# Optimization experiments

Measured on AMD Instinct MI355X. Metric: run time of the kernel, lower is better.

## Reference

```python
import jax, jax.numpy as jnp
import numpy as np

MAX_NUM_LEVELS = 3.5
NUM_LEVELS = 4  # mip levels 0..3 (levels clamped to [0, 2.5])


def affine_grid(matrix, N, H, W):
    # F.affine_grid, align_corners=False. matrix: (N,2,3) -> grid (N,H,W,2) in xy order.
    xs = (jnp.arange(W, dtype=jnp.float32) + 0.5) * (2.0 / W) - 1.0
    ys = (jnp.arange(H, dtype=jnp.float32) + 0.5) * (2.0 / H) - 1.0
    gy, gx = jnp.meshgrid(ys, xs, indexing='ij')
    base = jnp.stack([gx, gy, jnp.ones_like(gx)], axis=-1)  # (H,W,3)
    return jnp.einsum('hwk,nik->nhwi', base, matrix)  # (N,H,W,2)


def grid_sample_border(img, grid):
    # bilinear grid_sample, padding_mode='border', align_corners=False
    N, C, H, W = img.shape
    x = (grid[..., 0] + 1.0) * (W / 2.0) - 0.5
    y = (grid[..., 1] + 1.0) * (H / 2.0) - 0.5
    x0 = jnp.floor(x); y0 = jnp.floor(y)
    tx = x - x0; ty = y - y0
    x0i = jnp.clip(x0.astype(jnp.int32), 0, W - 1)
    x1i = jnp.clip(x0.astype(jnp.int32) + 1, 0, W - 1)
    y0i = jnp.clip(y0.astype(jnp.int32), 0, H - 1)
    y1i = jnp.clip(y0.astype(jnp.int32) + 1, 0, H - 1)
    b = jnp.arange(N)[:, None, None]
    g = lambda yi, xi: img[b, :, yi, xi]  # (N,Ho,Wo,C) gather
    out = (g(y0i, x0i) * ((1 - tx) * (1 - ty))[..., None]
           + g(y0i, x1i) * (tx * (1 - ty))[..., None]
           + g(y1i, x0i) * ((1 - tx) * ty)[..., None]
           + g(y1i, x1i) * (tx * ty)[..., None])
    return jnp.transpose(out, (0, 3, 1, 2))  # (N,C,Ho,Wo)


def blur_downsample(x):
    N, C, H, W = x.shape
    k1 = jnp.array([1., 3., 3., 1.], dtype=x.dtype) / 8.0
    k = k1[:, None] * k1[None, :]
    xp = jnp.pad(x, ((0, 0), (0, 0), (1, 2), (1, 2)), mode='reflect')
    kernel = jnp.broadcast_to(k[None, None], (C, 1, 4, 4))
    return jax.lax.conv_general_dilated(xp, kernel, window_strides=(2, 2), padding='VALID',
                                        feature_group_count=C,
                                        dimension_numbers=('NCHW', 'OIHW', 'NCHW'))


def compute_levels(grid, H, W):
    # per-pixel mip LOD from local stretch of the sampling grid (in source pixel units)
    coords = (grid + 1.0) * 0.5 * jnp.array([W, H], dtype=grid.dtype)  # (N,Ho,Wo,2)
    dx = coords[:, :-1, 1:] - coords[:, :-1, :-1]
    dy = coords[:, 1:, :-1] - coords[:, :-1, :-1]
    scale = jnp.maximum(jnp.linalg.norm(dx, axis=-1), jnp.linalg.norm(dy, axis=-1))
    scale = jnp.pad(scale, ((0, 0), (0, 1), (0, 1)), mode='edge')  # (N,Ho,Wo)
    levels = jnp.log2(jnp.maximum(scale, 1.0))
    return jnp.clip(levels, 0.0, MAX_NUM_LEVELS - 1.0)


def mipmap_warp(img, grid):
    N, C, H, W = img.shape
    levels = compute_levels(grid, H, W)  # (N,Ho,Wo)
    pyr = [img]
    for _ in range(NUM_LEVELS - 1):
        pyr.append(blur_downsample(pyr[-1]))
    samples = jnp.stack([grid_sample_border(p, grid) for p in pyr], axis=0)  # (L,N,C,Ho,Wo)
    ls = jnp.arange(NUM_LEVELS, dtype=levels.dtype)[:, None, None, None]
    w = jnp.clip(1.0 - jnp.abs(levels[None] - ls), 0.0, 1.0)  # trilinear blend weights (L,N,Ho,Wo)
    return jnp.einsum('lnhw,lnchw->nchw', w, samples)


def setup_inputs() -> dict:
    key = jax.random.key(0)
    k1, k2, k3 = jax.random.split(key, 3)
    N, C, H, W, D = 64, 3, 256, 256, 512
    img = jax.random.normal(k1, (N, C, H, W), dtype=jnp.float32)
    features = jax.random.normal(k2, (N, D), dtype=jnp.float32)
    # learned head params (zero-init in torch; small random here so the warp is nontrivial)
    lin_w = jax.random.normal(k3, (4, D), dtype=jnp.float32) * 0.02
    lin_b = jnp.zeros((4,), dtype=jnp.float32)
    return {'img': img, 'features': features, 'lin_w': lin_w, 'lin_b': lin_b}


def reference(img, features, lin_w, lin_b):
    params = features @ lin_w.T + lin_b  # (N,4)
    rot = jnp.tanh(params[:, 0:1]) * jnp.pi
    scale = jnp.exp(params[:, 1:2])
    sx, sy = params[:, 2:3], params[:, 3:4]
    c, s = jnp.cos(rot), jnp.sin(rot)
    matrix = jnp.concatenate([scale * c, -scale * s, sx, scale * s, scale * c, sy], axis=1).reshape(-1, 2, 3)
    affine_params = jnp.concatenate([rot, scale, sx, sy], axis=1)
    N, C, H, W = img.shape
    grid = affine_grid(matrix, N, H, W)
    out = mipmap_warp(img, grid)
    return out, grid, matrix, affine_params
```

## Files before the change

### kernel.cpp

```cpp
#include <hip/hip_runtime.h>
#include <math.h>

#define N_B 64
#define C_CH 3
#define H_IMG 256
#define W_IMG 256
#define D_FEAT 512

#define OUT_OFF_GRID   12582912
#define OUT_OFF_MATRIX 20971520
#define OUT_OFF_AFFINE 20971904

#define PYR1_SZ (N_B * 128 * 128 * 3)
#define PYR2_SZ (N_B * 64 * 64 * 3)
#define PYR3_SZ (N_B * 32 * 32 * 3)

typedef float v2f __attribute__((ext_vector_type(2)));
typedef float f4u __attribute__((ext_vector_type(4), aligned(4)));
typedef float f2u __attribute__((ext_vector_type(2), aligned(4)));

__global__ void params_kernel(const float* __restrict__ features,
                              const float* __restrict__ lin_w,
                              const float* __restrict__ lin_b,
                              float* __restrict__ out_matrix,
                              float* __restrict__ out_affine,
                              float* __restrict__ ws_params)
{
    const int n = blockIdx.x;
    const int t = threadIdx.x;
    const float* f = features + n * D_FEAT;
    float f0 = f[t];
    float f1 = f[t + 256];
    float a0 = f0 * lin_w[0 * D_FEAT + t] + f1 * lin_w[0 * D_FEAT + t + 256];
    float a1 = f0 * lin_w[1 * D_FEAT + t] + f1 * lin_w[1 * D_FEAT + t + 256];
    float a2 = f0 * lin_w[2 * D_FEAT + t] + f1 * lin_w[2 * D_FEAT + t + 256];
    float a3 = f0 * lin_w[3 * D_FEAT + t] + f1 * lin_w[3 * D_FEAT + t + 256];

    __shared__ float red[4][256];
    red[0][t] = a0; red[1][t] = a1; red[2][t] = a2; red[3][t] = a3;
    __syncthreads();
    for (int s = 128; s > 0; s >>= 1) {
        if (t < s) {
            red[0][t] += red[0][t + s];
            red[1][t] += red[1][t + s];
            red[2][t] += red[2][t + s];
            red[3][t] += red[3][t + s];
        }
        __syncthreads();
    }
    if (t == 0) {
        float p0 = red[0][0] + lin_b[0];
        float p1 = red[1][0] + lin_b[1];
        float p2 = red[2][0] + lin_b[2];
        float p3 = red[3][0] + lin_b[3];
        float rot   = tanhf(p0) * 3.14159265358979323846f;
        float scale = expf(p1);
        float c = cosf(rot), s = sinf(rot);
        float m00 = scale * c, m01 = -scale * s, m02 = p2;
        float m10 = scale * s, m11 =  scale * c, m12 = p3;
        out_matrix[n * 6 + 0] = m00;
        out_matrix[n * 6 + 1] = m01;
        out_matrix[n * 6 + 2] = m02;
        out_matrix[n * 6 + 3] = m10;
        out_matrix[n * 6 + 4] = m11;
        out_matrix[n * 6 + 5] = m12;
        out_affine[n * 4 + 0] = rot;
        out_affine[n * 4 + 1] = scale;
        out_affine[n * 4 + 2] = p2;
        out_affine[n * 4 + 3] = p3;
        float lv = log2f(fmaxf(scale, 1.0f));
        lv = fminf(fmaxf(lv, 0.0f), 2.5f);
        ws_params[n * 8 + 0] = m00;
        ws_params[n * 8 + 1] = m01;
        ws_params[n * 8 + 2] = m02;
        ws_params[n * 8 + 3] = m10;
        ws_params[n * 8 + 4] = m11;
        ws_params[n * 8 + 5] = m12;
        ws_params[n * 8 + 6] = lv;
        ws_params[n * 8 + 7] = 0.0f;
    }
}

__global__ void down1_kernel(const float* __restrict__ img,
                             float* __restrict__ pyr1,
                             const float* __restrict__ ws_params)
{
    const int n = blockIdx.y;
    if (ws_params[n * 8 + 6] <= 0.0f) return;
    const int idx = blockIdx.x * 256 + threadIdx.x;
    const int t = idx & 31;
    const int i = idx >> 5;

    int r[4];
#pragma unroll
    for (int a = 0; a < 4; a++) {
        int q = 2 * i + a - 1;
        if (q < 0) q = -q;
        if (q >= 256) q = 510 - q;
        r[a] = q;
    }
    const int c8 = 8 * t;
    const int li = (t > 0)  ? c8 - 1 : 1;
    const int ri = (t < 31) ? c8 + 8 : 254;

    const float* s = img + (size_t)n * 3 * 65536;

    const float k0 = 0.125f, k1 = 0.375f;
    const float kr[4] = {0.125f, 0.375f, 0.375f, 0.125f};

    float acc[3][4] = {};
#pragma unroll
    for (int a = 0; a < 4; a++) {
        const float* rbase = s + (size_t)r[a] * 256;
        f4u A[3], B[3];
        float L[3], R[3];
#pragma unroll
        for (int c = 0; c < 3; c++) {
            const float* row = rbase + c * 65536;
            A[c] = *(const f4u*)(row + c8);
            B[c] = *(const f4u*)(row + c8 + 4);
            L[c] = row[li];
            R[c] = row[ri];
        }
#pragma unroll
        for (int c = 0; c < 3; c++) {
            float h0 = k0 * L[c]   + k1 * A[c].x + k1 * A[c].y + k0 * A[c].z;
            float h1 = k0 * A[c].y + k1 * A[c].z + k1 * A[c].w + k0 * B[c].x;
            float h2 = k0 * A[c].w + k1 * B[c].x + k1 * B[c].y + k0 * B[c].z;
            float h3 = k0 * B[c].y + k1 * B[c].z + k1 * B[c].w + k0 * R[c];
            acc[c][0] += kr[a] * h0;
            acc[c][1] += kr[a] * h1;
            acc[c][2] += kr[a] * h2;
            acc[c][3] += kr[a] * h3;
        }
    }
    float* d = pyr1 + (size_t)n * (128 * 128 * 3) + ((size_t)i * 128 + 4 * t) * 3;
    f4u s0 = {acc[0][0], acc[1][0], acc[2][0], acc[0][1]};
    f4u s1 = {acc[1][1], acc[2][1], acc[0][2], acc[1][2]};
    f4u s2 = {acc[2][2], acc[0][3], acc[1][3], acc[2][3]};
    *(f4u*)(d)     = s0;
    *(f4u*)(d + 4) = s1;
    *(f4u*)(d + 8) = s2;
}

template<int Hs, int Ws>
__global__ void downN_kernel(const float* __restrict__ src,
                             float* __restrict__ dst,
                             const float* __restrict__ ws_params,
                             float lvl_gate)
{
    const int n = blockIdx.y;
    if (ws_params[n * 8 + 6] <= lvl_gate) return;
    constexpr int Hd = Hs / 2, Wd = Ws / 2;
    const int p = blockIdx.x * 256 + threadIdx.x;
    const int i = p / Wd;
    const int j = p % Wd;

    int r[4], cc[4];
#pragma unroll
    for (int a = 0; a < 4; a++) {
        int q = 2 * i + a - 1;
        if (q < 0) q = -q;
        if (q >= Hs) q = 2 * Hs - 2 - q;
        r[a] = q;
        int u = 2 * j + a - 1;
        if (u < 0) u = -u;
        if (u >= Ws) u = 2 * Ws - 2 - u;
        cc[a] = u;
    }
    const float* s = src + (size_t)n * 3 * Hs * Ws;
    const int rs = 3 * Ws;

    f4u T[4][4];
#pragma unroll
    for (int a = 0; a < 4; a++)
#pragma unroll
        for (int b = 0; b < 4; b++)
            T[a][b] = *(const f4u*)(s + r[a] * rs + 3 * cc[b]);

    const float k0 = 0.125f, k1 = 0.375f;
    const float kr[4] = {0.125f, 0.375f, 0.375f, 0.125f};
    float o[3];
#pragma unroll
    for (int c = 0; c < 3; c++) {
        float acc = 0.0f;
#pragma unroll
        for (int a = 0; a < 4; a++) {
            float h = k0 * T[a][0][c] + k1 * T[a][1][c]
                    + k1 * T[a][2][c] + k0 * T[a][3][c];
            acc += kr[a] * h;
        }
        o[c] = acc;
    }
    float* d = dst + (size_t)n * 3 * Hd * Wd + (size_t)p * 3;
    d[0] = o[0]; d[1] = o[1]; d[2] = o[2];
}

struct TapSetup {
    const float* row0;
    const float* row1;
    float w00, w01, w10, w11;
    bool selHi0, selLo1;
    size_t planeStride;
};

__device__ __forceinline__ TapSetup make_taps(const float* __restrict__ base, int l,
                                              float X, float Y)
{
    const int Wl = W_IMG >> l;
    const int Hl = H_IMG >> l;
    float x = (X + 1.0f) * (0.5f * (float)Wl) - 0.5f;
    float y = (Y + 1.0f) * (0.5f * (float)Hl) - 0.5f;
    float x0f = floorf(x), y0f = floorf(y);
    float tx = x - x0f, ty = y - y0f;
    int x0 = (int)x0f, y0 = (int)y0f;
    int y0i = min(max(y0,     0), Hl - 1);
    int y1i = min(max(y0 + 1, 0), Hl - 1);
    int xp = min(max(x0, 0), Wl - 2);
    TapSetup ts;
    ts.row0 = base + (size_t)y0i * Wl + xp;
    ts.row1 = base + (size_t)y1i * Wl + xp;
    ts.selHi0 = (x0 >= Wl - 1);
    ts.selLo1 = (x0 < 0);
    ts.w00 = (1.0f - tx) * (1.0f - ty);
    ts.w01 = tx * (1.0f - ty);
    ts.w10 = (1.0f - tx) * ty;
    ts.w11 = tx * ty;
    ts.planeStride = (size_t)Hl * Wl;
    return ts;
}

__device__ __forceinline__ float tap_eval(const TapSetup& ts, float2 a, float2 b)
{
    float t00 = ts.selHi0 ? a.y : a.x;
    float t01 = ts.selLo1 ? a.x : a.y;
    float t10 = ts.selHi0 ? b.y : b.x;
    float t11 = ts.selLo1 ? b.x : b.y;
    return ts.w00 * t00 + ts.w01 * t01 + ts.w10 * t10 + ts.w11 * t11;
}

struct NTap {
    const float* r0;
    const float* r1;
    float w00, w01, w10, w11;
    bool hi, lo;
};

__device__ __forceinline__ NTap make_ntap(const float* __restrict__ base, int l,
                                          float X, float Y)
{
    const int Wl = W_IMG >> l;
    const int Hl = H_IMG >> l;
    float x = (X + 1.0f) * (0.5f * (float)Wl) - 0.5f;
    float y = (Y + 1.0f) * (0.5f * (float)Hl) - 0.5f;
    float x0f = floorf(x), y0f = floorf(y);
    float tx = x - x0f, ty = y - y0f;
    int x0 = (int)x0f, y0 = (int)y0f;
    int y0i = min(max(y0,     0), Hl - 1);
    int y1i = min(max(y0 + 1, 0), Hl - 1);
    int xp  = min(max(x0, 0), Wl - 2);
    const int rs = 3 * Wl;
    NTap t;
    t.r0 = base + (size_t)y0i * rs + 3 * xp;
    t.r1 = base + (size_t)y1i * rs + 3 * xp;
    t.hi = (x0 >= Wl - 1);
    t.lo = (x0 < 0);
    t.w00 = (1.0f - tx) * (1.0f - ty);
    t.w01 = tx * (1.0f - ty);
    t.w10 = (1.0f - tx) * ty;
    t.w11 = tx * ty;
    return t;
}

struct NPay { f4u a; f2u a2; f4u b; f2u b2; };

__device__ __forceinline__ NPay ntap_load(const NTap& t)
{
    NPay p;
    p.a  = *(const f4u*)t.r0;  p.a2 = *(const f2u*)(t.r0 + 4);
    p.b  = *(const f4u*)t.r1;  p.b2 = *(const f2u*)(t.r1 + 4);
    return p;
}

__device__ __forceinline__ void ntap_eval(const NTap& t, const NPay& p, float* v)
{
    float e0[6] = {p.a.x, p.a.y, p.a.z, p.a.w, p.a2.x, p.a2.y};
    float e1[6] = {p.b.x, p.b.y, p.b.z, p.b.w, p.b2.x, p.b2.y};
#pragma unroll
    for (int c = 0; c < 3; c++) {
        float p00 = t.hi ? e0[c + 3] : e0[c];
        float p01 = t.lo ? e0[c]     : e0[c + 3];
        float p10 = t.hi ? e1[c + 3] : e1[c];
        float p11 = t.lo ? e1[c]     : e1[c + 3];
        v[c] = t.w00 * p00 + t.w01 * p01 + t.w10 * p10 + t.w11 * p11;
    }
}

__device__ __forceinline__ const float* npyr(int l, const float* p1,
                                             const float* p2, const float* p3,
                                             int n)
{
    if (l == 1) return p1 + (size_t)n * (128 * 128 * 3);
    if (l == 2) return p2 + (size_t)n * (64 * 64 * 3);
    return p3 + (size_t)n * (32 * 32 * 3);
}

__global__ __launch_bounds__(256, 4)
void warp_kernel(const float* __restrict__ img,
                 const float* __restrict__ pyr1,
                 const float* __restrict__ pyr2,
                 const float* __restrict__ pyr3,
                 const float* __restrict__ ws_params,
                 float* __restrict__ out,
                 float* __restrict__ gridOut)
{
    const int n = blockIdx.y;
    const int tile = blockIdx.x;
    const int tid = threadIdx.x;
    const int w0 = (tile & 7) << 5;
    const int h0 = (tile >> 3) << 4;
    const int w  = w0 + (((tid >> 6) & 1) << 4) + (tid & 15);
    const int ha = h0 + ((tid >> 7) << 2) + ((tid >> 4) & 3);
    const int hb = ha + 8;

    const float* P = ws_params + n * 8;
    float m00 = P[0], m01 = P[1], m02 = P[2];
    float m10 = P[3], m11 = P[4], m12 = P[5];
    float lv  = P[6];

    float gx  = ((float)w + 0.5f) * (2.0f / (float)W_IMG) - 1.0f;
    float gya = ((float)ha + 0.5f) * (2.0f / (float)H_IMG) - 1.0f;
    float gyb = ((float)hb + 0.5f) * (2.0f / (float)H_IMG) - 1.0f;
    float Xa = m00 * gx + m01 * gya + m02;
    float Ya = m10 * gx + m11 * gya + m12;
    float Xb = m00 * gx + m01 * gyb + m02;
    float Yb = m10 * gx + m11 * gyb + m12;

    v2f gpa = {Xa, Ya}, gpb = {Xb, Yb};
    __builtin_nontemporal_store(gpa, (v2f*)gridOut + ((size_t)(n * H_IMG + ha) * W_IMG + w));
    __builtin_nontemporal_store(gpb, (v2f*)gridOut + ((size_t)(n * H_IMG + hb) * W_IMG + w));

    int   l0   = (int)lv;
    float frac = lv - (float)l0;
    const bool hasL1 = (frac > 0.0f);
    const float wA = 1.0f - frac;

    size_t oba = ((size_t)n * C_CH * H_IMG + ha) * W_IMG + w;
    size_t obb = ((size_t)n * C_CH * H_IMG + hb) * W_IMG + w;

    if (l0 == 0) {
        const float* base0 = img + (size_t)n * 3 * 65536;
        TapSetup ta = make_taps(base0, 0, Xa, Ya);
        TapSetup tb = make_taps(base0, 0, Xb, Yb);
        float2 Aa[3], Ba[3], Ab[3], Bb[3];
#pragma unroll
        for (int c = 0; c < 3; c++) {
            Aa[c] = *(const float2*)(ta.row0 + c * 65536);
            Ba[c] = *(const float2*)(ta.row1 + c * 65536);
        }
#pragma unroll
        for (int c = 0; c < 3; c++) {
            Ab[c] = *(const float2*)(tb.row0 + c * 65536);
            Bb[c] = *(const float2*)(tb.row1 + c * 65536);
        }
        if (hasL1) {
            const float* b1 = pyr1 + (size_t)n * (128 * 128 * 3);
            NTap ua = make_ntap(b1, 1, Xa, Ya);
            NTap ub = make_ntap(b1, 1, Xb, Yb);
            NPay pa = ntap_load(ua);
            NPay pb = ntap_load(ub);
            float v1a[3], v1b[3];
            ntap_eval(ua, pa, v1a);
            ntap_eval(ub, pb, v1b);
#pragma unroll
            for (int c = 0; c < 3; c++) {
                float v0a = tap_eval(ta, Aa[c], Ba[c]);
                float v0b = tap_eval(tb, Ab[c], Bb[c]);
                __builtin_nontemporal_store(wA * v0a + frac * v1a[c],
                                            out + oba + (size_t)c * 65536);
                __builtin_nontemporal_store(wA * v0b + frac * v1b[c],
                                            out + obb + (size_t)c * 65536);
            }
        } else {
#pragma unroll
            for (int c = 0; c < 3; c++) {
                __builtin_nontemporal_store(tap_eval(ta, Aa[c], Ba[c]),
                                            out + oba + (size_t)c * 65536);
                __builtin_nontemporal_store(tap_eval(tb, Ab[c], Bb[c]),
                                            out + obb + (size_t)c * 65536);
            }
        }
    } else {
        const float* base0 = npyr(l0, pyr1, pyr2, pyr3, n);
        NTap ta = make_ntap(base0, l0, Xa, Ya);
        NTap tb = make_ntap(base0, l0, Xb, Yb);
        NPay pa = ntap_load(ta);
        NPay pb = ntap_load(tb);
        if (hasL1) {
            const float* base1 = npyr(l0 + 1, pyr1, pyr2, pyr3, n);
            NTap ua = make_ntap(base1, l0 + 1, Xa, Ya);
            NTap ub = make_ntap(base1, l0 + 1, Xb, Yb);
            NPay qa = ntap_load(ua);
            NPay qb = ntap_load(ub);
            float v0a[3], v0b[3], v1a[3], v1b[3];
            ntap_eval(ta, pa, v0a);
            ntap_eval(tb, pb, v0b);
            ntap_eval(ua, qa, v1a);
            ntap_eval(ub, qb, v1b);
#pragma unroll
            for (int c = 0; c < 3; c++) {
                __builtin_nontemporal_store(wA * v0a[c] + frac * v1a[c],
                                            out + oba + (size_t)c * 65536);
                __builtin_nontemporal_store(wA * v0b[c] + frac * v1b[c],
                                            out + obb + (size_t)c * 65536);
            }
        } else {
            float v0a[3], v0b[3];
            ntap_eval(ta, pa, v0a);
            ntap_eval(tb, pb, v0b);
#pragma unroll
            for (int c = 0; c < 3; c++) {
                __builtin_nontemporal_store(v0a[c], out + oba + (size_t)c * 65536);
                __builtin_nontemporal_store(v0b[c], out + obb + (size_t)c * 65536);
            }
        }
    }
}

extern "C" void kernel_launch(void* const* d_in, const int* in_sizes, int n_in,
                              void* d_out, int out_size, void* d_ws, size_t ws_size,
                              hipStream_t stream)
{
    const float* img      = (const float*)d_in[0];
    const float* features = (const float*)d_in[1];
    const float* lin_w    = (const float*)d_in[2];
    const float* lin_b    = (const float*)d_in[3];

    float* out        = (float*)d_out;
    float* gridOut    = out + OUT_OFF_GRID;
    float* out_matrix = out + OUT_OFF_MATRIX;
    float* out_affine = out + OUT_OFF_AFFINE;

    float* ws        = (float*)d_ws;
    float* ws_params = ws;
    float* pyr1 = ws + 1024;
    float* pyr2 = pyr1 + PYR1_SZ;
    float* pyr3 = pyr2 + PYR2_SZ;

    params_kernel<<<N_B, 256, 0, stream>>>(features, lin_w, lin_b,
                                           out_matrix, out_affine, ws_params);

    down1_kernel<<<dim3(16, N_B), 256, 0, stream>>>(img, pyr1, ws_params);
    downN_kernel<128, 128><<<dim3(16, N_B), 256, 0, stream>>>(pyr1, pyr2, ws_params, 1.0f);
    downN_kernel<64, 64><<<dim3(4, N_B), 256, 0, stream>>>(pyr2, pyr3, ws_params, 2.0f);

    warp_kernel<<<dim3(H_IMG * W_IMG / 512, N_B), 256, 0, stream>>>(
        img, pyr1, pyr2, pyr3, ws_params, out, gridOut);
}
```

Baseline: 173.6 us.

## Remap down1 to one output pixel per thread and pair horizontal pixels in warp

The first downsample kernel now gives each thread a single output pixel instead of four, quadrupling the grid. Each thread reads one 4-wide window per row and channel and picks taps through edge-case selects. The warp kernel now has each thread handle two horizontally adjacent pixels rather than two pixels eight rows apart, so grid and image outputs go out as wider vector stores. This trades redundant overlapping loads and more threads in down1 for extra parallelism, and in warp changes tap locality and store width.

```diff
diff --git a/kernel.cpp b/kernel.cpp
--- a/kernel.cpp
+++ b/kernel.cpp
@@ -16,6 +16,7 @@
 #define PYR3_SZ (N_B * 32 * 32 * 3)
 
 typedef float v2f __attribute__((ext_vector_type(2)));
+typedef float v4f __attribute__((ext_vector_type(4)));
 typedef float f4u __attribute__((ext_vector_type(4), aligned(4)));
 typedef float f2u __attribute__((ext_vector_type(2), aligned(4)));
 
@@ -87,9 +88,9 @@
 {
     const int n = blockIdx.y;
     if (ws_params[n * 8 + 6] <= 0.0f) return;
-    const int idx = blockIdx.x * 256 + threadIdx.x;
-    const int t = idx & 31;
-    const int i = idx >> 5;
+    const int p = blockIdx.x * 256 + threadIdx.x;
+    const int i = p >> 7;
+    const int j = p & 127;
 
     int r[4];
 #pragma unroll
@@ -99,48 +100,40 @@
         if (q >= 256) q = 510 - q;
         r[a] = q;
     }
-    const int c8 = 8 * t;
-    const int li = (t > 0)  ? c8 - 1 : 1;
-    const int ri = (t < 31) ? c8 + 8 : 254;
+    const int  cb  = min(max(2 * j - 1, 0), 252);
+    const bool jlo = (j == 0);
+    const bool jhi = (j == 127);
+    const bool je  = jlo || jhi;
 
     const float* s = img + (size_t)n * 3 * 65536;
+
+    f4u T[3][4];
+#pragma unroll
+    for (int c = 0; c < 3; c++)
+#pragma unroll
+        for (int a = 0; a < 4; a++)
+            T[c][a] = *(const f4u*)(s + c * 65536 + r[a] * 256 + cb);
 
     const float k0 = 0.125f, k1 = 0.375f;
     const float kr[4] = {0.125f, 0.375f, 0.375f, 0.125f};
-
-    float acc[3][4] = {};
-#pragma unroll
-    for (int a = 0; a < 4; a++) {
-        const float* rbase = s + (size_t)r[a] * 256;
-        f4u A[3], B[3];
-        float L[3], R[3];
-#pragma unroll
-        for (int c = 0; c < 3; c++) {
-            const float* row = rbase + c * 65536;
-            A[c] = *(const f4u*)(row + c8);
-            B[c] = *(const f4u*)(row + c8 + 4);
-            L[c] = row[li];
-            R[c] = row[ri];
-        }
-#pragma unroll
-        for (int c = 0; c < 3; c++) {
-            float h0 = k0 * L[c]   + k1 * A[c].x + k1 * A[c].y + k0 * A[c].z;
-            float h1 = k0 * A[c].y + k1 * A[c].z + k1 * A[c].w + k0 * B[c].x;
-            float h2 = k0 * A[c].w + k1 * B[c].x + k1 * B[c].y + k0 * B[c].z;
-            float h3 = k0 * B[c].y + k1 * B[c].z + k1 * B[c].w + k0 * R[c];
-            acc[c][0] += kr[a] * h0;
-            acc[c][1] += kr[a] * h1;
-            acc[c][2] += kr[a] * h2;
-            acc[c][3] += kr[a] * h3;
-        }
-    }
-    float* d = pyr1 + (size_t)n * (128 * 128 * 3) + ((size_t)i * 128 + 4 * t) * 3;
-    f4u s0 = {acc[0][0], acc[1][0], acc[2][0], acc[0][1]};
-    f4u s1 = {acc[1][1], acc[2][1], acc[0][2], acc[1][2]};
-    f4u s2 = {acc[2][2], acc[0][3], acc[1][3], acc[2][3]};
-    *(f4u*)(d)     = s0;
-    *(f4u*)(d + 4) = s1;
-    *(f4u*)(d + 8) = s2;
+    float o[3];
+#pragma unroll
+    for (int c = 0; c < 3; c++) {
+        float acc = 0.0f;
+#pragma unroll
+        for (int a = 0; a < 4; a++) {
+            f4u A = T[c][a];
+            float t0 = je  ? A.y : A.x;
+            float t1 = jlo ? A.x : (jhi ? A.z : A.y);
+            float t2 = jlo ? A.y : (jhi ? A.w : A.z);
+            float t3 = je  ? A.z : A.w;
+            float h = k0 * t0 + k1 * t1 + k1 * t2 + k0 * t3;
+            acc += kr[a] * h;
+        }
+        o[c] = acc;
+    }
+    float* d = pyr1 + (size_t)n * (128 * 128 * 3) + (size_t)p * 3;
+    d[0] = o[0]; d[1] = o[1]; d[2] = o[2];
 }
 
 template<int Hs, int Ws>
@@ -319,34 +312,32 @@
     const int tid = threadIdx.x;
     const int w0 = (tile & 7) << 5;
     const int h0 = (tile >> 3) << 4;
-    const int w  = w0 + (((tid >> 6) & 1) << 4) + (tid & 15);
-    const int ha = h0 + ((tid >> 7) << 2) + ((tid >> 4) & 3);
-    const int hb = ha + 8;
+    const int w  = w0 + ((tid & 15) << 1);
+    const int h  = h0 + (tid >> 4);
 
     const float* P = ws_params + n * 8;
     float m00 = P[0], m01 = P[1], m02 = P[2];
     float m10 = P[3], m11 = P[4], m12 = P[5];
     float lv  = P[6];
 
-    float gx  = ((float)w + 0.5f) * (2.0f / (float)W_IMG) - 1.0f;
-    float gya = ((float)ha + 0.5f) * (2.0f / (float)H_IMG) - 1.0f;
-    float gyb = ((float)hb + 0.5f) * (2.0f / (float)H_IMG) - 1.0f;
-    float Xa = m00 * gx + m01 * gya + m02;
-    float Ya = m10 * gx + m11 * gya + m12;
-    float Xb = m00 * gx + m01 * gyb + m02;
-    float Yb = m10 * gx + m11 * gyb + m12;
-
-    v2f gpa = {Xa, Ya}, gpb = {Xb, Yb};
-    __builtin_nontemporal_store(gpa, (v2f*)gridOut + ((size_t)(n * H_IMG + ha) * W_IMG + w));
-    __builtin_nontemporal_store(gpb, (v2f*)gridOut + ((size_t)(n * H_IMG + hb) * W_IMG + w));
+    float gxa = ((float)w + 0.5f) * (2.0f / (float)W_IMG) - 1.0f;
+    float gxb = ((float)(w + 1) + 0.5f) * (2.0f / (float)W_IMG) - 1.0f;
+    float gy  = ((float)h + 0.5f) * (2.0f / (float)H_IMG) - 1.0f;
+    float Xa = m00 * gxa + m01 * gy + m02;
+    float Ya = m10 * gxa + m11 * gy + m12;
+    float Xb = m00 * gxb + m01 * gy + m02;
+    float Yb = m10 * gxb + m11 * gy + m12;
+
+    v4f gp = {Xa, Ya, Xb, Yb};
+    __builtin_nontemporal_store(gp,
+        (v4f*)(gridOut + ((size_t)(n * H_IMG + h) * W_IMG + w) * 2));
 
     int   l0   = (int)lv;
     float frac = lv - (float)l0;
     const bool hasL1 = (frac > 0.0f);
     const float wA = 1.0f - frac;
 
-    size_t oba = ((size_t)n * C_CH * H_IMG + ha) * W_IMG + w;
-    size_t obb = ((size_t)n * C_CH * H_IMG + hb) * W_IMG + w;
+    size_t obase = ((size_t)n * C_CH * H_IMG + h) * W_IMG + w;
 
     if (l0 == 0) {
         const float* base0 = img + (size_t)n * 3 * 65536;
@@ -357,9 +348,6 @@
         for (int c = 0; c < 3; c++) {
             Aa[c] = *(const float2*)(ta.row0 + c * 65536);
             Ba[c] = *(const float2*)(ta.row1 + c * 65536);
-        }
-#pragma unroll
-        for (int c = 0; c < 3; c++) {
             Ab[c] = *(const float2*)(tb.row0 + c * 65536);
             Bb[c] = *(const float2*)(tb.row1 + c * 65536);
         }
@@ -376,18 +364,16 @@
             for (int c = 0; c < 3; c++) {
                 float v0a = tap_eval(ta, Aa[c], Ba[c]);
                 float v0b = tap_eval(tb, Ab[c], Bb[c]);
-                __builtin_nontemporal_store(wA * v0a + frac * v1a[c],
-                                            out + oba + (size_t)c * 65536);
-                __builtin_nontemporal_store(wA * v0b + frac * v1b[c],
-                                            out + obb + (size_t)c * 65536);
+                v2f o2 = {wA * v0a + frac * v1a[c], wA * v0b + frac * v1b[c]};
+                __builtin_nontemporal_store(o2,
+                    (v2f*)(out + obase + (size_t)c * 65536));
             }
         } else {
 #pragma unroll
             for (int c = 0; c < 3; c++) {
-                __builtin_nontemporal_store(tap_eval(ta, Aa[c], Ba[c]),
-                                            out + oba + (size_t)c * 65536);
-                __builtin_nontemporal_store(tap_eval(tb, Ab[c], Bb[c]),
-                                            out + obb + (size_t)c * 65536);
+                v2f o2 = {tap_eval(ta, Aa[c], Ba[c]), tap_eval(tb, Ab[c], Bb[c])};
+                __builtin_nontemporal_store(o2,
+                    (v2f*)(out + obase + (size_t)c * 65536));
             }
         }
     } else {
@@ -409,10 +395,9 @@
             ntap_eval(ub, qb, v1b);
 #pragma unroll
             for (int c = 0; c < 3; c++) {
-                __builtin_nontemporal_store(wA * v0a[c] + frac * v1a[c],
-                                            out + oba + (size_t)c * 65536);
-                __builtin_nontemporal_store(wA * v0b[c] + frac * v1b[c],
-                                            out + obb + (size_t)c * 65536);
+                v2f o2 = {wA * v0a[c] + frac * v1a[c], wA * v0b[c] + frac * v1b[c]};
+                __builtin_nontemporal_store(o2,
+                    (v2f*)(out + obase + (size_t)c * 65536));
             }
         } else {
             float v0a[3], v0b[3];
@@ -420,8 +405,9 @@
             ntap_eval(tb, pb, v0b);
 #pragma unroll
             for (int c = 0; c < 3; c++) {
-                __builtin_nontemporal_store(v0a[c], out + oba + (size_t)c * 65536);
-                __builtin_nontemporal_store(v0b[c], out + obb + (size_t)c * 65536);
+                v2f o2 = {v0a[c], v0b[c]};
+                __builtin_nontemporal_store(o2,
+                    (v2f*)(out + obase + (size_t)c * 65536));
             }
         }
     }
@@ -450,7 +436,7 @@
     params_kernel<<<N_B, 256, 0, stream>>>(features, lin_w, lin_b,
                                            out_matrix, out_affine, ws_params);
 
-    down1_kernel<<<dim3(16, N_B), 256, 0, stream>>>(img, pyr1, ws_params);
+    down1_kernel<<<dim3(64, N_B), 256, 0, stream>>>(img, pyr1, ws_params);
     downN_kernel<128, 128><<<dim3(16, N_B), 256, 0, stream>>>(pyr1, pyr2, ws_params, 1.0f);
     downN_kernel<64, 64><<<dim3(4, N_B), 256, 0, stream>>>(pyr2, pyr3, ws_params, 2.0f);
 
```

Measured after the change: 164.5 us. 5.2% less time.
